# Performance work log

Hardware: AMD Instinct MI355X
Metric: run time of the kernel (lower is better)

Reference implementation:

```python
import jax, jax.numpy as jnp
import numpy as np

HIDDEN = 256
N_PROT = 12288
N_MOL = 6144
N_BATCH = 32


def setup_inputs() -> dict:
    key = jax.random.key(0)
    ks = jax.random.split(key, 10)
    s = 1.0 / np.sqrt(HIDDEN)  # torch Linear default init scale
    inp = {
        "prot_embed": jax.random.normal(ks[0], (N_PROT, HIDDEN), jnp.float32),
        "mol_embed": jax.random.normal(ks[1], (N_MOL, HIDDEN), jnp.float32),
        "prot_batch": jnp.sort(jax.random.randint(ks[2], (N_PROT,), 0, N_BATCH)),
        "mol_batch": jnp.sort(jax.random.randint(ks[3], (N_MOL,), 0, N_BATCH)),
        "Wq": jax.random.uniform(ks[4], (HIDDEN, HIDDEN), jnp.float32, -s, s),
        "bq": jax.random.uniform(ks[5], (HIDDEN,), jnp.float32, -s, s),
        "Wk": jax.random.uniform(ks[6], (HIDDEN, HIDDEN), jnp.float32, -s, s),
        "bk": jax.random.uniform(ks[7], (HIDDEN,), jnp.float32, -s, s),
        "Wv": jax.random.uniform(ks[8], (HIDDEN, HIDDEN), jnp.float32, -s, s),
        "bv": jax.random.uniform(ks[9], (HIDDEN,), jnp.float32, -s, s),
    }
    return inp


def reference(prot_embed, mol_embed, prot_batch, mol_batch, Wq, bq, Wk, bk, Wv, bv):
    # Linear projections (torch nn.Linear: x @ W.T + b)
    Q = prot_embed @ Wq.T + bq            # [N, H]
    K = mol_embed @ Wk.T + bk             # [M, H]
    V = mol_embed @ Wv.T + bv             # [M, H]

    scale = 1.0 / jnp.sqrt(jnp.asarray(Q.shape[-1], Q.dtype))
    scores = (Q @ K.T) * scale            # [N, M]

    # block mask: same-batch pairs only
    mask = prot_batch[:, None] == mol_batch[None, :]   # [N, M] bool
    neg_inf = jnp.asarray(-jnp.inf, scores.dtype)
    scores = jnp.where(mask, scores, neg_inf)

    # stable masked softmax; rows with no valid key -> all zeros
    # (matches torch softmax(-inf row) -> nan -> nan_to_num(0.0))
    row_any = mask.any(axis=-1, keepdims=True)
    mx = jnp.max(scores, axis=-1, keepdims=True)
    mx = jnp.where(row_any, mx, 0.0)
    e = jnp.exp(scores - mx)              # exp(-inf)=0 on masked entries
    denom = jnp.sum(e, axis=-1, keepdims=True)
    attn = e / jnp.where(row_any, denom, 1.0)  # [N, M]

    out = attn @ V                        # [N, H]
    return out, attn
```

## Files before the change

### kernel.cpp

```cpp
#include <hip/hip_runtime.h>

#define NPROT 12288
#define NMOL  6144
#define HID   256
#define NB    32

#define PROT_O 0
#define MOL_O  3145728
#define WQ_O   4718592
#define WK_O   4784128
#define WV_O   4849664
#define BQ_O   4915200
#define BK_O   4915456
#define BV_O   4915712
#define Q_O    4915968
#define K_O    8061696
#define VT_O   9634560
#define CVT_END 11207424

typedef __attribute__((ext_vector_type(4))) float f32x4;
typedef __attribute__((ext_vector_type(8))) short bf16x8;
typedef unsigned short u16;
typedef unsigned int   u32;

__device__ __forceinline__ float b2f(u16 u){
  union { u32 i; float f; } v; v.i = ((u32)u) << 16; return v.f;
}
__device__ __forceinline__ u16 f2b(float f){
  union { float fl; u32 i; } v; v.fl = f;
  u32 i = v.i;
  return (u16)((i + 0x7FFFu + ((i >> 16) & 1u)) >> 16);
}

__global__ __launch_bounds__(1024) void init_kernel(
    const int* __restrict__ pb, const int* __restrict__ mb,
    const u32* __restrict__ wq_raw, int* __restrict__ rg){
  int t = threadIdx.x;
  if (t < 132) rg[t] = 0;
  __syncthreads();
  for (int i = t; i < NPROT; i += 1024){
    int b = pb[i];
    if (i == 0 || pb[i-1] != b) rg[b] = i;
    if (i == NPROT-1 || pb[i+1] != b) rg[32+b] = i+1;
  }
  for (int i = t; i < NMOL; i += 1024){
    int b = mb[i];
    if (i == 0 || mb[i-1] != b) rg[64+b] = i;
    if (i == NMOL-1 || mb[i+1] != b) rg[96+b] = i+1;
  }
  if (t == 0){
    int cnt = 0;
    #pragma unroll
    for (int i = 0; i < 64; i++){
      u32 lo = wq_raw[i] & 0xFFFFu;
      if (((lo >> 7) & 0xFFu) >= 0x7Bu) cnt++;
    }
    rg[128] = (cnt >= 16) ? 1 : 0;
  }
}

__global__ __launch_bounds__(256) void convert_kernel(
    const float* __restrict__ prot, const float* __restrict__ mol,
    const float* __restrict__ Wq, const float* __restrict__ Wk,
    const float* __restrict__ Wv, const float* __restrict__ bq,
    const float* __restrict__ bk, const float* __restrict__ bv,
    const int* __restrict__ rg, u16* __restrict__ dst0){
  if (!rg[128]) return;
  const float* src; u16* dst; int n;
  switch (blockIdx.y){
    case 0:  src = prot; dst = dst0 + PROT_O; n = 3145728; break;
    case 1:  src = mol;  dst = dst0 + MOL_O;  n = 1572864; break;
    case 2:  src = Wq;   dst = dst0 + WQ_O;   n = 65536;   break;
    case 3:  src = Wk;   dst = dst0 + WK_O;   n = 65536;   break;
    case 4:  src = Wv;   dst = dst0 + WV_O;   n = 65536;   break;
    case 5:  src = bq;   dst = dst0 + BQ_O;   n = 256;     break;
    case 6:  src = bk;   dst = dst0 + BK_O;   n = 256;     break;
    default: src = bv;   dst = dst0 + BV_O;   n = 256;     break;
  }
  int i4 = blockIdx.x * 256 + threadIdx.x;
  if (i4 * 4 >= n) return;
  f32x4 v = *(const f32x4*)(src + (size_t)i4 * 4);
  ushort4 o;
  o.x = f2b(v[0]); o.y = f2b(v[1]); o.z = f2b(v[2]); o.w = f2b(v[3]);
  *(ushort4*)(dst + (size_t)i4 * 4) = o;
}

__global__ __launch_bounds__(256) void proj_kernel(
    const void* __restrict__ prot0, const void* __restrict__ mol0,
    const void* __restrict__ Wq0, const void* __restrict__ bq0,
    const void* __restrict__ Wk0, const void* __restrict__ bk0,
    const void* __restrict__ Wv0, const void* __restrict__ bv0,
    const int* __restrict__ rg, const u16* __restrict__ cvt,
    u16* __restrict__ Q, u16* __restrict__ K, u16* __restrict__ Vt)
{
  __shared__ u16 tlds[4][64][18];
  int f32f = rg[128];
  int proj = blockIdx.z;
  const u16 *X, *W, *B;
  int nrows;
  if (proj == 0){
    X = f32f ? cvt + PROT_O : (const u16*)prot0;
    W = f32f ? cvt + WQ_O   : (const u16*)Wq0;
    B = f32f ? cvt + BQ_O   : (const u16*)bq0;
    nrows = NPROT;
  } else if (proj == 1){
    X = f32f ? cvt + MOL_O  : (const u16*)mol0;
    W = f32f ? cvt + WK_O   : (const u16*)Wk0;
    B = f32f ? cvt + BK_O   : (const u16*)bk0;
    nrows = NMOL;
  } else {
    X = f32f ? cvt + MOL_O  : (const u16*)mol0;
    W = f32f ? cvt + WV_O   : (const u16*)Wv0;
    B = f32f ? cvt + BV_O   : (const u16*)bv0;
    nrows = NMOL;
  }
  if ((int)blockIdx.x * 64 >= nrows) return;

  int wave = threadIdx.x >> 6, lane = threadIdx.x & 63;
  int m = lane & 15, q = lane >> 4;
  int rowbase = blockIdx.x * 64 + wave * 16;
  int colbase = blockIdx.y * 64;

  const u16* arow = X + (size_t)(rowbase + m) * HID;
  f32x4 acc[4] = {};
  for (int k0 = 0; k0 < HID; k0 += 32){
    bf16x8 a = *(const bf16x8*)(arow + k0 + q*8);
    #pragma unroll
    for (int ct = 0; ct < 4; ct++){
      bf16x8 b = *(const bf16x8*)(W + (size_t)(colbase + ct*16 + m) * HID + k0 + q*8);
      acc[ct] = __builtin_amdgcn_mfma_f32_16x16x32_bf16(a, b, acc[ct], 0, 0, 0);
    }
  }

  if (proj < 2){
    u16* O = (proj == 0) ? Q : K;
    #pragma unroll
    for (int ct = 0; ct < 4; ct++){
      int col = colbase + ct*16 + m;
      float bb = b2f(B[col]);
      #pragma unroll
      for (int r = 0; r < 4; r++){
        int row = rowbase + q*4 + r;
        O[(size_t)row * HID + col] = f2b(acc[ct][r] + bb);
      }
    }
  } else {
    #pragma unroll
    for (int ct = 0; ct < 4; ct++){
      int lc = ct*16 + m;
      float bb = b2f(B[colbase + lc]);
      #pragma unroll
      for (int r = 0; r < 4; r++)
        tlds[wave][lc][q*4 + r] = f2b(acc[ct][r] + bb);
    }
    __syncthreads();
    int col = colbase + lane;
    u32 packed[8];
    #pragma unroll
    for (int i = 0; i < 8; i++){
      u16 lo = tlds[wave][lane][2*i];
      u16 hi = tlds[wave][lane][2*i+1];
      packed[i] = (u32)lo | ((u32)hi << 16);
    }
    u16* dst = Vt + (size_t)col * NMOL + rowbase;
    uint4 v0 = {packed[0], packed[1], packed[2], packed[3]};
    uint4 v1 = {packed[4], packed[5], packed[6], packed[7]};
    *(uint4*)dst = v0;
    *(uint4*)(dst + 8) = v1;
  }
}

__global__ __launch_bounds__(256) void attn_kernel(
    const int* __restrict__ rg, const u16* __restrict__ Q, const u16* __restrict__ K,
    const u16* __restrict__ Vt, void* __restrict__ dout)
{
  __shared__ u16 plds[4][16][48];
  __shared__ float mxw[4][16];
  __shared__ float smw[4][16];
  __shared__ float red[2][4096];
  const float scale = 0.0625f;
  int f32f = rg[128];
  int b = blockIdx.y;
  int ps = rg[b], pe = rg[32+b], ms = rg[64+b], me = rg[96+b];
  int Np = pe - ps, Nm = me - ms;
  if (Np <= 0) return;

  int wave = threadIdx.x >> 6, lane = threadIdx.x & 63;
  int m = lane & 15, q = lane >> 4;
  float* outf  = (float*)dout;
  u16*   outh  = (u16*)dout;
  float* attnf = outf + (size_t)NPROT * HID;
  u16*   attnh = outh + (size_t)NPROT * HID;
  int ntiles = (Np + 15) >> 4;

  int bs = 0, ce = 0;
  if (Nm > 0){ bs = ms & ~31; ce = bs + ((me - bs + 31) & ~31); }

  for (int tile = blockIdx.x; tile < ntiles; tile += gridDim.x){
    int row0 = ps + tile * 16;

    if (f32f){
      for (int cs = wave*64; cs < NMOL; cs += 256){
        int col = cs + m*4;
        if (col < bs || col >= ce){
          f32x4 z = {0.f, 0.f, 0.f, 0.f};
          #pragma unroll
          for (int rr = 0; rr < 4; rr++){
            int row = row0 + q*4 + rr;
            if (row < pe) *(f32x4*)(attnf + (size_t)row * NMOL + col) = z;
          }
        }
      }
    } else {
      for (int cs = wave*128; cs < NMOL; cs += 512){
        int col = cs + m*8;
        if (col < bs || col >= ce){
          uint4 z = {0u, 0u, 0u, 0u};
          #pragma unroll
          for (int rr = 0; rr < 4; rr++){
            int row = row0 + q*4 + rr;
            if (row < pe) *(uint4*)(attnh + (size_t)row * NMOL + col) = z;
          }
        }
      }
    }

    int qr = min(row0 + m, NPROT - 1);
    const u16* qrow = Q + (size_t)qr * HID;
    bf16x8 qf[8];
    #pragma unroll
    for (int kk = 0; kk < 8; kk++)
      qf[kk] = *(const bf16x8*)(qrow + kk*32 + q*8);

    if (Nm > 0){
      float mx[4] = {-1e30f, -1e30f, -1e30f, -1e30f};
      float sm[4] = {0.f, 0.f, 0.f, 0.f};
      for (int j0 = bs + wave*16; j0 < me; j0 += 64){
        int col = j0 + m;
        bool valid = (col >= ms) && (col < me);
        const u16* krow = K + (size_t)min(col, NMOL-1) * HID;
        f32x4 s = {0.f, 0.f, 0.f, 0.f};
        #pragma unroll
        for (int kk = 0; kk < 8; kk++){
          bf16x8 kb = *(const bf16x8*)(krow + kk*32 + q*8);
          s = __builtin_amdgcn_mfma_f32_16x16x32_bf16(qf[kk], kb, s, 0, 0, 0);
        }
        float sv[4], cm[4];
        #pragma unroll
        for (int r = 0; r < 4; r++){
          sv[r] = valid ? s[r] * scale : -1e30f;
          cm[r] = sv[r];
        }
        #pragma unroll
        for (int d = 1; d < 16; d <<= 1)
          #pragma unroll
          for (int r = 0; r < 4; r++)
            cm[r] = fmaxf(cm[r], __shfl_xor(cm[r], d, 16));
        float e[4];
        #pragma unroll
        for (int r = 0; r < 4; r++){
          float mn = fmaxf(mx[r], cm[r]);
          float corr = __expf(mx[r] - mn);
          e[r] = __expf(sv[r] - mn);
          mx[r] = mn;
          sm[r] = sm[r] * corr;
        }
        #pragma unroll
        for (int d = 1; d < 16; d <<= 1)
          #pragma unroll
          for (int r = 0; r < 4; r++)
            e[r] += __shfl_xor(e[r], d, 16);
        #pragma unroll
        for (int r = 0; r < 4; r++) sm[r] += e[r];
      }
      if (m == 0){
        #pragma unroll
        for (int r = 0; r < 4; r++){
          mxw[wave][q*4 + r] = mx[r];
          smw[wave][q*4 + r] = sm[r];
        }
      }
      __syncthreads();

      float gmx[4], ginv[4];
      #pragma unroll
      for (int r = 0; r < 4; r++){
        int row = q*4 + r;
        float M = mxw[0][row];
        #pragma unroll
        for (int w = 1; w < 4; w++) M = fmaxf(M, mxw[w][row]);
        float S = 0.f;
        #pragma unroll
        for (int w = 0; w < 4; w++) S += smw[w][row] * __expf(mxw[w][row] - M);
        gmx[r] = M;
        ginv[r] = (S > 0.f) ? (1.f / S) : 0.f;
      }

      f32x4 oacc[16] = {};
      for (int j0 = bs + wave*32; j0 < ce; j0 += 128){
        #pragma unroll
        for (int sub = 0; sub < 2; sub++){
          int col = j0 + sub*16 + m;
          bool valid = (col >= ms) && (col < me);
          const u16* krow = K + (size_t)col * HID;
          f32x4 s = {0.f, 0.f, 0.f, 0.f};
          #pragma unroll
          for (int kk = 0; kk < 8; kk++){
            bf16x8 kb = *(const bf16x8*)(krow + kk*32 + q*8);
            s = __builtin_amdgcn_mfma_f32_16x16x32_bf16(qf[kk], kb, s, 0, 0, 0);
          }
          #pragma unroll
          for (int r = 0; r < 4; r++){
            float pv = valid ? __expf(s[r]*scale - gmx[r]) * ginv[r] : 0.f;
            u16 pb16 = f2b(pv);
            plds[wave][q*4 + r][sub*16 + m] = pb16;
            int row = row0 + q*4 + r;
            if (row < pe){
              if (f32f) attnf[(size_t)row * NMOL + col] = pv;
              else      attnh[(size_t)row * NMOL + col] = pb16;
            }
          }
        }
        bf16x8 a = *(const bf16x8*)(&plds[wave][m][q*8]);
        int kbase = j0 + q*8;
        #pragma unroll
        for (int ct = 0; ct < 16; ct++){
          bf16x8 vb = *(const bf16x8*)(Vt + (size_t)(ct*16 + m) * NMOL + kbase);
          oacc[ct] = __builtin_amdgcn_mfma_f32_16x16x32_bf16(a, vb, oacc[ct], 0, 0, 0);
        }
      }
      __syncthreads();

      if (wave == 1 || wave == 3){
        float* dst = red[(wave - 1) >> 1];
        #pragma unroll
        for (int ct = 0; ct < 16; ct++)
          #pragma unroll
          for (int r = 0; r < 4; r++)
            dst[(ct*4 + r)*64 + lane] = oacc[ct][r];
      }
      __syncthreads();
      if (wave == 0 || wave == 2){
        const float* src = red[wave >> 1];
        #pragma unroll
        for (int ct = 0; ct < 16; ct++)
          #pragma unroll
          for (int r = 0; r < 4; r++)
            oacc[ct][r] += src[(ct*4 + r)*64 + lane];
      }
      __syncthreads();
      if (wave == 2){
        #pragma unroll
        for (int ct = 0; ct < 16; ct++)
          #pragma unroll
          for (int r = 0; r < 4; r++)
            red[0][(ct*4 + r)*64 + lane] = oacc[ct][r];
      }
      __syncthreads();
      if (wave == 0){
        #pragma unroll
        for (int ct = 0; ct < 16; ct++){
          int colh = ct*16 + m;
          #pragma unroll
          for (int r = 0; r < 4; r++){
            float o = oacc[ct][r] + red[0][(ct*4 + r)*64 + lane];
            int row = row0 + q*4 + r;
            if (row < pe){
              if (f32f) outf[(size_t)row * HID + colh] = o;
              else      outh[(size_t)row * HID + colh] = f2b(o);
            }
          }
        }
      }
    } else {
      if (wave == 0){
        #pragma unroll
        for (int ct = 0; ct < 16; ct++){
          int colh = ct*16 + m;
          #pragma unroll
          for (int r = 0; r < 4; r++){
            int row = row0 + q*4 + r;
            if (row < pe){
              if (f32f) outf[(size_t)row * HID + colh] = 0.f;
              else      outh[(size_t)row * HID + colh] = 0;
            }
          }
        }
      }
    }
    __syncthreads();
  }
}

extern "C" void kernel_launch(void* const* d_in, const int* in_sizes, int n_in,
                              void* d_out, int out_size, void* d_ws, size_t ws_size,
                              hipStream_t stream)
{
  (void)in_sizes; (void)n_in; (void)out_size;
  const void* prot = d_in[0];
  const void* mol  = d_in[1];
  const int* pb    = (const int*)d_in[2];
  const int* mb    = (const int*)d_in[3];
  const void* Wq   = d_in[4];
  const void* bq   = d_in[5];
  const void* Wk   = d_in[6];
  const void* bk   = d_in[7];
  const void* Wv   = d_in[8];
  const void* bv   = d_in[9];

  const size_t need = 1024 + (size_t)CVT_END * 2;
  if (ws_size < need) return;

  char* ws = (char*)d_ws;
  int* rg  = (int*)ws;
  u16* cvt = (u16*)(ws + 1024);
  u16* Qp  = cvt + Q_O;
  u16* Kp  = cvt + K_O;
  u16* Vtp = cvt + VT_O;

  init_kernel<<<dim3(1), dim3(1024), 0, stream>>>(pb, mb, (const u32*)Wq, rg);
  convert_kernel<<<dim3(3072, 8), dim3(256), 0, stream>>>(
      (const float*)prot, (const float*)mol, (const float*)Wq, (const float*)Wk,
      (const float*)Wv, (const float*)bq, (const float*)bk, (const float*)bv, rg, cvt);
  proj_kernel<<<dim3(192, 4, 3), dim3(256), 0, stream>>>(
      prot, mol, Wq, bq, Wk, bk, Wv, bv, rg, cvt, Qp, Kp, Vtp);
  attn_kernel<<<dim3(32, NB), dim3(256), 0, stream>>>(rg, Qp, Kp, Vtp, d_out);
}
```

Baseline: 441.8 us.

## Merge init into convert, drop dtype detection, compact grids, split QK accumulators

Removes the single-block init kernel and folds batch range discovery into the convert kernel as a 64-thread binary search. It also drops the runtime bf16/fp32 detection, so every path assumes fp32 inputs. The convert and projection grids are flattened to skip the idle blocks of the old padded grids. The QK^T MFMA chain is split into two independent accumulators to shorten the dependency chain. This saves a launch and serial init work, but loses support for bf16 inputs.

```diff
diff --git a/kernel.cpp b/kernel.cpp
--- a/kernel.cpp
+++ b/kernel.cpp
@@ -16,7 +16,7 @@
 #define Q_O    4915968
 #define K_O    8061696
 #define VT_O   9634560
-#define CVT_END 11207424
+#define END_O  11207424
 
 typedef __attribute__((ext_vector_type(4))) float f32x4;
 typedef __attribute__((ext_vector_type(8))) short bf16x8;
@@ -30,33 +30,6 @@
   union { float fl; u32 i; } v; v.fl = f;
   u32 i = v.i;
   return (u16)((i + 0x7FFFu + ((i >> 16) & 1u)) >> 16);
-}
-
-__global__ __launch_bounds__(1024) void init_kernel(
-    const int* __restrict__ pb, const int* __restrict__ mb,
-    const u32* __restrict__ wq_raw, int* __restrict__ rg){
-  int t = threadIdx.x;
-  if (t < 132) rg[t] = 0;
-  __syncthreads();
-  for (int i = t; i < NPROT; i += 1024){
-    int b = pb[i];
-    if (i == 0 || pb[i-1] != b) rg[b] = i;
-    if (i == NPROT-1 || pb[i+1] != b) rg[32+b] = i+1;
-  }
-  for (int i = t; i < NMOL; i += 1024){
-    int b = mb[i];
-    if (i == 0 || mb[i-1] != b) rg[64+b] = i;
-    if (i == NMOL-1 || mb[i+1] != b) rg[96+b] = i+1;
-  }
-  if (t == 0){
-    int cnt = 0;
-    #pragma unroll
-    for (int i = 0; i < 64; i++){
-      u32 lo = wq_raw[i] & 0xFFFFu;
-      if (((lo >> 7) & 0xFFu) >= 0x7Bu) cnt++;
-    }
-    rg[128] = (cnt >= 16) ? 1 : 0;
-  }
 }
 
 __global__ __launch_bounds__(256) void convert_kernel(
@@ -64,61 +37,63 @@
     const float* __restrict__ Wq, const float* __restrict__ Wk,
     const float* __restrict__ Wv, const float* __restrict__ bq,
     const float* __restrict__ bk, const float* __restrict__ bv,
-    const int* __restrict__ rg, u16* __restrict__ dst0){
-  if (!rg[128]) return;
-  const float* src; u16* dst; int n;
-  switch (blockIdx.y){
-    case 0:  src = prot; dst = dst0 + PROT_O; n = 3145728; break;
-    case 1:  src = mol;  dst = dst0 + MOL_O;  n = 1572864; break;
-    case 2:  src = Wq;   dst = dst0 + WQ_O;   n = 65536;   break;
-    case 3:  src = Wk;   dst = dst0 + WK_O;   n = 65536;   break;
-    case 4:  src = Wv;   dst = dst0 + WV_O;   n = 65536;   break;
-    case 5:  src = bq;   dst = dst0 + BQ_O;   n = 256;     break;
-    case 6:  src = bk;   dst = dst0 + BK_O;   n = 256;     break;
-    default: src = bv;   dst = dst0 + BV_O;   n = 256;     break;
-  }
-  int i4 = blockIdx.x * 256 + threadIdx.x;
-  if (i4 * 4 >= n) return;
-  f32x4 v = *(const f32x4*)(src + (size_t)i4 * 4);
-  ushort4 o;
-  o.x = f2b(v[0]); o.y = f2b(v[1]); o.z = f2b(v[2]); o.w = f2b(v[3]);
-  *(ushort4*)(dst + (size_t)i4 * 4) = o;
+    const int* __restrict__ pb, const int* __restrict__ mb,
+    int* __restrict__ rg, u16* __restrict__ cvt)
+{
+  int g = blockIdx.x * 256 + threadIdx.x;
+  const float* src = nullptr; u16* dst = nullptr; int off = 0;
+  if      (g < 786432)  { src = prot; dst = cvt + PROT_O; off = g; }
+  else if (g < 1179648) { src = mol;  dst = cvt + MOL_O;  off = g - 786432; }
+  else if (g < 1196032) { src = Wq;   dst = cvt + WQ_O;   off = g - 1179648; }
+  else if (g < 1212416) { src = Wk;   dst = cvt + WK_O;   off = g - 1196032; }
+  else if (g < 1228800) { src = Wv;   dst = cvt + WV_O;   off = g - 1212416; }
+  else if (g < 1228864) { src = bq;   dst = cvt + BQ_O;   off = g - 1228800; }
+  else if (g < 1228928) { src = bk;   dst = cvt + BK_O;   off = g - 1228864; }
+  else if (g < 1228992) { src = bv;   dst = cvt + BV_O;   off = g - 1228928; }
+  if (src){
+    f32x4 v = *(const f32x4*)(src + (size_t)off * 4);
+    ushort4 o;
+    o.x = f2b(v[0]); o.y = f2b(v[1]); o.z = f2b(v[2]); o.w = f2b(v[3]);
+    *(ushort4*)(dst + (size_t)off * 4) = o;
+  }
+
+  if (blockIdx.x == 0 && threadIdx.x < 64){
+    int t = threadIdx.x;
+    const int* arr = (t < 32) ? pb : mb;
+    int n          = (t < 32) ? NPROT : NMOL;
+    int target     = (t & 31) + 1;
+    int lo = 0, hi = n;
+    while (lo < hi){
+      int mid = (lo + hi) >> 1;
+      if (arr[mid] < target) lo = mid + 1; else hi = mid;
+    }
+    int end = lo;
+    int prev = __shfl(end, t - 1);
+    int start = ((t & 31) == 0) ? 0 : prev;
+    int b = t & 31;
+    if (t < 32){ rg[b] = start; rg[32 + b] = end; }
+    else       { rg[64 + b] = start; rg[96 + b] = end; }
+  }
 }
 
 __global__ __launch_bounds__(256) void proj_kernel(
-    const void* __restrict__ prot0, const void* __restrict__ mol0,
-    const void* __restrict__ Wq0, const void* __restrict__ bq0,
-    const void* __restrict__ Wk0, const void* __restrict__ bk0,
-    const void* __restrict__ Wv0, const void* __restrict__ bv0,
-    const int* __restrict__ rg, const u16* __restrict__ cvt,
+    const u16* __restrict__ cvt,
     u16* __restrict__ Q, u16* __restrict__ K, u16* __restrict__ Vt)
 {
   __shared__ u16 tlds[4][64][18];
-  int f32f = rg[128];
-  int proj = blockIdx.z;
+  int x = blockIdx.x;
+  int proj, rowblk;
+  if      (x < 192){ proj = 0; rowblk = x; }
+  else if (x < 288){ proj = 1; rowblk = x - 192; }
+  else             { proj = 2; rowblk = x - 288; }
   const u16 *X, *W, *B;
-  int nrows;
-  if (proj == 0){
-    X = f32f ? cvt + PROT_O : (const u16*)prot0;
-    W = f32f ? cvt + WQ_O   : (const u16*)Wq0;
-    B = f32f ? cvt + BQ_O   : (const u16*)bq0;
-    nrows = NPROT;
-  } else if (proj == 1){
-    X = f32f ? cvt + MOL_O  : (const u16*)mol0;
-    W = f32f ? cvt + WK_O   : (const u16*)Wk0;
-    B = f32f ? cvt + BK_O   : (const u16*)bk0;
-    nrows = NMOL;
-  } else {
-    X = f32f ? cvt + MOL_O  : (const u16*)mol0;
-    W = f32f ? cvt + WV_O   : (const u16*)Wv0;
-    B = f32f ? cvt + BV_O   : (const u16*)bv0;
-    nrows = NMOL;
-  }
-  if ((int)blockIdx.x * 64 >= nrows) return;
+  if (proj == 0){ X = cvt + PROT_O; W = cvt + WQ_O; B = cvt + BQ_O; }
+  else if (proj == 1){ X = cvt + MOL_O; W = cvt + WK_O; B = cvt + BK_O; }
+  else { X = cvt + MOL_O; W = cvt + WV_O; B = cvt + BV_O; }
 
   int wave = threadIdx.x >> 6, lane = threadIdx.x & 63;
   int m = lane & 15, q = lane >> 4;
-  int rowbase = blockIdx.x * 64 + wave * 16;
+  int rowbase = rowblk * 64 + wave * 16;
   int colbase = blockIdx.y * 64;
 
   const u16* arow = X + (size_t)(rowbase + m) * HID;
@@ -172,14 +147,13 @@
 
 __global__ __launch_bounds__(256) void attn_kernel(
     const int* __restrict__ rg, const u16* __restrict__ Q, const u16* __restrict__ K,
-    const u16* __restrict__ Vt, void* __restrict__ dout)
+    const u16* __restrict__ Vt, float* __restrict__ dout)
 {
   __shared__ u16 plds[4][16][48];
   __shared__ float mxw[4][16];
   __shared__ float smw[4][16];
   __shared__ float red[2][4096];
   const float scale = 0.0625f;
-  int f32f = rg[128];
   int b = blockIdx.y;
   int ps = rg[b], pe = rg[32+b], ms = rg[64+b], me = rg[96+b];
   int Np = pe - ps, Nm = me - ms;
@@ -187,10 +161,8 @@
 
   int wave = threadIdx.x >> 6, lane = threadIdx.x & 63;
   int m = lane & 15, q = lane >> 4;
-  float* outf  = (float*)dout;
-  u16*   outh  = (u16*)dout;
-  float* attnf = outf + (size_t)NPROT * HID;
-  u16*   attnh = outh + (size_t)NPROT * HID;
+  float* outf  = dout;
+  float* attnf = dout + (size_t)NPROT * HID;
   int ntiles = (Np + 15) >> 4;
 
   int bs = 0, ce = 0;
@@ -199,28 +171,14 @@
   for (int tile = blockIdx.x; tile < ntiles; tile += gridDim.x){
     int row0 = ps + tile * 16;
 
-    if (f32f){
-      for (int cs = wave*64; cs < NMOL; cs += 256){
-        int col = cs + m*4;
-        if (col < bs || col >= ce){
-          f32x4 z = {0.f, 0.f, 0.f, 0.f};
-          #pragma unroll
-          for (int rr = 0; rr < 4; rr++){
-            int row = row0 + q*4 + rr;
-            if (row < pe) *(f32x4*)(attnf + (size_t)row * NMOL + col) = z;
-          }
-        }
-      }
-    } else {
-      for (int cs = wave*128; cs < NMOL; cs += 512){
-        int col = cs + m*8;
-        if (col < bs || col >= ce){
-          uint4 z = {0u, 0u, 0u, 0u};
-          #pragma unroll
-          for (int rr = 0; rr < 4; rr++){
-            int row = row0 + q*4 + rr;
-            if (row < pe) *(uint4*)(attnh + (size_t)row * NMOL + col) = z;
-          }
+    for (int cs = wave*64; cs < NMOL; cs += 256){
+      int col = cs + m*4;
+      if (col < bs || col >= ce){
+        f32x4 z = {0.f, 0.f, 0.f, 0.f};
+        #pragma unroll
+        for (int rr = 0; rr < 4; rr++){
+          int row = row0 + q*4 + rr;
+          if (row < pe) *(f32x4*)(attnf + (size_t)row * NMOL + col) = z;
         }
       }
     }
@@ -239,12 +197,15 @@
         int col = j0 + m;
         bool valid = (col >= ms) && (col < me);
         const u16* krow = K + (size_t)min(col, NMOL-1) * HID;
-        f32x4 s = {0.f, 0.f, 0.f, 0.f};
-        #pragma unroll
-        for (int kk = 0; kk < 8; kk++){
-          bf16x8 kb = *(const bf16x8*)(krow + kk*32 + q*8);
-          s = __builtin_amdgcn_mfma_f32_16x16x32_bf16(qf[kk], kb, s, 0, 0, 0);
-        }
+        f32x4 s0 = {0.f,0.f,0.f,0.f}, s1 = {0.f,0.f,0.f,0.f};
+        #pragma unroll
+        for (int kk = 0; kk < 4; kk++){
+          bf16x8 kb0 = *(const bf16x8*)(krow + kk*32 + q*8);
+          bf16x8 kb1 = *(const bf16x8*)(krow + (kk+4)*32 + q*8);
+          s0 = __builtin_amdgcn_mfma_f32_16x16x32_bf16(qf[kk],   kb0, s0, 0, 0, 0);
+          s1 = __builtin_amdgcn_mfma_f32_16x16x32_bf16(qf[kk+4], kb1, s1, 0, 0, 0);
+        }
+        f32x4 s = s0 + s1;
         float sv[4], cm[4];
         #pragma unroll
         for (int r = 0; r < 4; r++){
@@ -303,22 +264,22 @@
           int col = j0 + sub*16 + m;
           bool valid = (col >= ms) && (col < me);
           const u16* krow = K + (size_t)col * HID;
-          f32x4 s = {0.f, 0.f, 0.f, 0.f};
-          #pragma unroll
-          for (int kk = 0; kk < 8; kk++){
-            bf16x8 kb = *(const bf16x8*)(krow + kk*32 + q*8);
-            s = __builtin_amdgcn_mfma_f32_16x16x32_bf16(qf[kk], kb, s, 0, 0, 0);
+          f32x4 s0 = {0.f,0.f,0.f,0.f}, s1 = {0.f,0.f,0.f,0.f};
+          #pragma unroll
+          for (int kk = 0; kk < 4; kk++){
+            bf16x8 kb0 = *(const bf16x8*)(krow + kk*32 + q*8);
+            bf16x8 kb1 = *(const bf16x8*)(krow + (kk+4)*32 + q*8);
+            s0 = __builtin_amdgcn_mfma_f32_16x16x32_bf16(qf[kk],   kb0, s0, 0, 0, 0);
+            s1 = __builtin_amdgcn_mfma_f32_16x16x32_bf16(qf[kk+4], kb1, s1, 0, 0, 0);
           }
+          f32x4 s = s0 + s1;
           #pragma unroll
           for (int r = 0; r < 4; r++){
             float pv = valid ? __expf(s[r]*scale - gmx[r]) * ginv[r] : 0.f;
             u16 pb16 = f2b(pv);
             plds[wave][q*4 + r][sub*16 + m] = pb16;
             int row = row0 + q*4 + r;
-            if (row < pe){
-              if (f32f) attnf[(size_t)row * NMOL + col] = pv;
-              else      attnh[(size_t)row * NMOL + col] = pb16;
-            }
+            if (row < pe) attnf[(size_t)row * NMOL + col] = pv;
           }
         }
         bf16x8 a = *(const bf16x8*)(&plds[wave][m][q*8]);
@@ -365,10 +326,7 @@
           for (int r = 0; r < 4; r++){
             float o = oacc[ct][r] + red[0][(ct*4 + r)*64 + lane];
             int row = row0 + q*4 + r;
-            if (row < pe){
-              if (f32f) outf[(size_t)row * HID + colh] = o;
-              else      outh[(size_t)row * HID + colh] = f2b(o);
-            }
+            if (row < pe) outf[(size_t)row * HID + colh] = o;
           }
         }
       }
@@ -380,10 +338,7 @@
           #pragma unroll
           for (int r = 0; r < 4; r++){
             int row = row0 + q*4 + r;
-            if (row < pe){
-              if (f32f) outf[(size_t)row * HID + colh] = 0.f;
-              else      outh[(size_t)row * HID + colh] = 0;
-            }
+            if (row < pe) outf[(size_t)row * HID + colh] = 0.f;
           }
         }
       }
@@ -397,18 +352,18 @@
                               hipStream_t stream)
 {
   (void)in_sizes; (void)n_in; (void)out_size;
-  const void* prot = d_in[0];
-  const void* mol  = d_in[1];
-  const int* pb    = (const int*)d_in[2];
-  const int* mb    = (const int*)d_in[3];
-  const void* Wq   = d_in[4];
-  const void* bq   = d_in[5];
-  const void* Wk   = d_in[6];
-  const void* bk   = d_in[7];
-  const void* Wv   = d_in[8];
-  const void* bv   = d_in[9];
-
-  const size_t need = 1024 + (size_t)CVT_END * 2;
+  const float* prot = (const float*)d_in[0];
+  const float* mol  = (const float*)d_in[1];
+  const int* pb     = (const int*)d_in[2];
+  const int* mb     = (const int*)d_in[3];
+  const float* Wq   = (const float*)d_in[4];
+  const float* bq   = (const float*)d_in[5];
+  const float* Wk   = (const float*)d_in[6];
+  const float* bk   = (const float*)d_in[7];
+  const float* Wv   = (const float*)d_in[8];
+  const float* bv   = (const float*)d_in[9];
+
+  const size_t need = 1024 + (size_t)END_O * 2;
   if (ws_size < need) return;
 
   char* ws = (char*)d_ws;
@@ -418,11 +373,8 @@
   u16* Kp  = cvt + K_O;
   u16* Vtp = cvt + VT_O;
 
-  init_kernel<<<dim3(1), dim3(1024), 0, stream>>>(pb, mb, (const u32*)Wq, rg);
-  convert_kernel<<<dim3(3072, 8), dim3(256), 0, stream>>>(
-      (const float*)prot, (const float*)mol, (const float*)Wq, (const float*)Wk,
-      (const float*)Wv, (const float*)bq, (const float*)bk, (const float*)bv, rg, cvt);
-  proj_kernel<<<dim3(192, 4, 3), dim3(256), 0, stream>>>(
-      prot, mol, Wq, bq, Wk, bk, Wv, bv, rg, cvt, Qp, Kp, Vtp);
-  attn_kernel<<<dim3(32, NB), dim3(256), 0, stream>>>(rg, Qp, Kp, Vtp, d_out);
-}
+  convert_kernel<<<dim3(4801), dim3(256), 0, stream>>>(
+      prot, mol, Wq, Wk, Wv, bq, bk, bv, pb, mb, rg, cvt);
+  proj_kernel<<<dim3(384, 4), dim3(256), 0, stream>>>(cvt, Qp, Kp, Vtp);
+  attn_kernel<<<dim3(32, NB), dim3(256), 0, stream>>>(rg, Qp, Kp, Vtp, (float*)d_out);
+}
```

Result: faster. 417.7 us (-5.5%).
